# Kernel tuning notes

Hardware: AMD Instinct MI355X
Metric: run time of the kernel (lower is better)

The kernel has to match this reference:

```python
import jax, jax.numpy as jnp
import numpy as np

D_MODEL = 1024
NUM_HEADS = 16
D_K = D_MODEL // NUM_HEADS
THETA = 10000.0
B, T = 4, 2048


def apply_rope(x, positions):
    # x: [B, h, T, d_k], positions: [B, T] int
    half = D_K // 2
    inv_freq = 1.0 / (THETA ** (jnp.arange(half, dtype=jnp.float32) * 2.0 / D_K))  # [half]
    ang = positions.astype(jnp.float32)[:, None, :, None] * inv_freq  # [B,1,T,half]
    cos, sin = jnp.cos(ang), jnp.sin(ang)
    x1, x2 = x[..., 0::2], x[..., 1::2]  # even/odd interleaved pairs
    r1 = x1 * cos - x2 * sin
    r2 = x1 * sin + x2 * cos
    return jnp.stack([r1, r2], axis=-1).reshape(x.shape)


def setup_inputs() -> dict:
    key = jax.random.key(0)
    ks = jax.random.split(key, 5)
    scale = 1.0 / np.sqrt(D_MODEL)
    return {
        "in_features": jax.random.normal(ks[0], (B, T, D_MODEL), dtype=jnp.float32),
        "token_positions": jnp.broadcast_to(jnp.arange(T, dtype=jnp.int64), (B, T)),
        "Wq": jax.random.normal(ks[1], (D_MODEL, D_MODEL), dtype=jnp.float32) * scale,
        "Wk": jax.random.normal(ks[2], (D_MODEL, D_MODEL), dtype=jnp.float32) * scale,
        "Wv": jax.random.normal(ks[3], (D_MODEL, D_MODEL), dtype=jnp.float32) * scale,
        "Wo": jax.random.normal(ks[4], (D_MODEL, D_MODEL), dtype=jnp.float32) * scale,
    }


def reference(in_features, token_positions, Wq, Wk, Wv, Wo):
    x = in_features  # [B, T, d_model]
    # Linear stores weight [out, in]; y = x @ W.T (no bias)
    def proj(W):
        y = jnp.einsum('btd,ed->bte', x, W)
        return y.reshape(B, T, NUM_HEADS, D_K).transpose(0, 2, 1, 3)  # [B,h,T,d_k]
    Q, K, V = proj(Wq), proj(Wk), proj(Wv)
    Q = apply_rope(Q, token_positions)
    K = apply_rope(K, token_positions)
    scores = jnp.einsum('bhqd,bhkd->bhqk', Q, K) / jnp.sqrt(jnp.float32(D_K))
    causal = jnp.tril(jnp.ones((T, T), dtype=bool))  # True where allowed
    scores = jnp.where(causal, scores, jnp.float32(-1e30))
    attn = jax.nn.softmax(scores, axis=-1)
    heads = jnp.einsum('bhqk,bhkd->bhqd', attn, V)  # [B,h,T,d_k]
    out = heads.transpose(0, 2, 1, 3).reshape(B, T, D_MODEL)
    return jnp.einsum('btd,ed->bte', out, Wo)
```

## Files before the change

### kernel.cpp

```cpp
#include <hip/hip_runtime.h>
#include <cstdint>
#include <cstddef>

typedef unsigned short ushort_t;
typedef __attribute__((ext_vector_type(8))) short short8;
typedef __attribute__((ext_vector_type(4))) float f32x4;
typedef __attribute__((ext_vector_type(4))) _Float16 half4;
struct half4x2 { half4 lo, hi; };

__device__ __forceinline__ unsigned short f2bf(float f) {
    unsigned u = __float_as_uint(f);
    u += 0x7fffu + ((u >> 16) & 1u);
    return (unsigned short)(u >> 16);
}
__device__ __forceinline__ float bf2f(unsigned short h) {
    return __uint_as_float((unsigned)h << 16);
}
__device__ __forceinline__ ushort_t f2h(float f) {
    _Float16 h = (_Float16)f;
    return __builtin_bit_cast(unsigned short, h);
}
__device__ __forceinline__ f32x4 zero4() {
    f32x4 z; z[0]=0.f; z[1]=0.f; z[2]=0.f; z[3]=0.f; return z;
}
__device__ __forceinline__ void gld_lds16(const ushort_t* g, ushort_t* l) {
    __builtin_amdgcn_global_load_lds(
        (const __attribute__((address_space(1))) void*)g,
        (__attribute__((address_space(3))) void*)l, 16, 0, 0);
}

__global__ void cvt_all(const float* __restrict__ x,
                        const float* __restrict__ wq, const float* __restrict__ wk,
                        const float* __restrict__ wv, const float* __restrict__ wo,
                        ushort_t* __restrict__ xb,
                        ushort_t* __restrict__ wqb, ushort_t* __restrict__ wkb,
                        ushort_t* __restrict__ wvb, ushort_t* __restrict__ wob) {
    int idx = blockIdx.x * 256 + threadIdx.x;
    const float* src; ushort_t* dst; int off;
    if (idx < 2097152) { src = x; dst = xb; off = idx; }
    else {
        int r = idx - 2097152;
        int w = r >> 18;
        off = r & 262143;
        src = (w == 0) ? wq : (w == 1) ? wk : (w == 2) ? wv : wo;
        dst = (w == 0) ? wqb : (w == 1) ? wkb : (w == 2) ? wvb : wob;
    }
    float4 v = ((const float4*)src)[off];
    ushort_t o[4];
    o[0] = f2bf(v.x); o[1] = f2bf(v.y); o[2] = f2bf(v.z); o[3] = f2bf(v.w);
    *(ushort4*)(dst + 4*(size_t)off) = *(const ushort4*)o;
}

__device__ __forceinline__ void gemm_core(const ushort_t* __restrict__ A,
                                          const ushort_t* __restrict__ W,
                                          ushort_t* As, ushort_t* Bs,
                                          int m0, int n0, f32x4 (&acc)[4][4]) {
    const int tid  = threadIdx.x;
    const int wave = tid >> 6, lane = tid & 63;
    const int wm = (wave >> 1) * 64, wn = (wave & 1) * 64;
    const int lrow = lane >> 2, lcol = (lane & 3) * 8;
    const int q = lane >> 4, c = lane & 15;

    const ushort_t* ag0 = A + (size_t)(m0 + wave*16 + lrow) * 1024 + lcol;
    const ushort_t* ag1 = A + (size_t)(m0 + 64 + wave*16 + lrow) * 1024 + lcol;
    const ushort_t* bg0 = W + (size_t)(n0 + wave*16 + lrow) * 1024 + lcol;
    const ushort_t* bg1 = W + (size_t)(n0 + 64 + wave*16 + lrow) * 1024 + lcol;
    ushort_t* al0 = As + wave*512;
    ushort_t* al1 = As + 2048 + wave*512;
    ushort_t* bl0 = Bs + wave*512;
    ushort_t* bl1 = Bs + 2048 + wave*512;

    for (int k0 = 0; k0 < 1024; k0 += 32) {
        __syncthreads();
        gld_lds16(ag0 + k0, al0);
        gld_lds16(ag1 + k0, al1);
        gld_lds16(bg0 + k0, bl0);
        gld_lds16(bg1 + k0, bl1);
        asm volatile("s_waitcnt vmcnt(0)" ::: "memory");
        __syncthreads();

        short8 af[4], bf[4];
#pragma unroll
        for (int i = 0; i < 4; ++i)
            af[i] = *(const short8*)(As + (wm + i*16 + c)*32 + q*8);
#pragma unroll
        for (int j = 0; j < 4; ++j)
            bf[j] = *(const short8*)(Bs + (wn + j*16 + c)*32 + q*8);
#pragma unroll
        for (int i = 0; i < 4; ++i)
#pragma unroll
            for (int j = 0; j < 4; ++j)
                acc[i][j] = __builtin_amdgcn_mfma_f32_16x16x32_bf16(af[i], bf[j], acc[i][j], 0, 0, 0);
    }
}

__global__ __launch_bounds__(256) void gemm_qkv_kernel(
    const ushort_t* __restrict__ X, const ushort_t* __restrict__ Wq,
    const ushort_t* __restrict__ Wk, const ushort_t* __restrict__ Wv,
    ushort_t* __restrict__ Q, ushort_t* __restrict__ K, ushort_t* __restrict__ V) {
    __shared__ ushort_t As[128*32];
    __shared__ ushort_t Bs[128*32];
    const int which = blockIdx.z;
    const ushort_t* W = (which == 0) ? Wq : (which == 1) ? Wk : Wv;
    ushort_t* OUT    = (which == 0) ? Q  : (which == 1) ? K  : V;
    const int m0 = blockIdx.y * 128, n0 = blockIdx.x * 128;

    f32x4 acc[4][4];
#pragma unroll
    for (int i = 0; i < 4; ++i)
#pragma unroll
        for (int j = 0; j < 4; ++j) acc[i][j] = zero4();

    gemm_core(X, W, As, Bs, m0, n0, acc);

    const int lane = threadIdx.x & 63, wave = threadIdx.x >> 6;
    const int q = lane >> 4, c = lane & 15;
    const int wm = (wave >> 1) * 64, wn = (wave & 1) * 64;
#pragma unroll
    for (int i = 0; i < 4; ++i)
#pragma unroll
        for (int j = 0; j < 4; ++j)
#pragma unroll
            for (int r = 0; r < 4; ++r) {
                int mm = m0 + wm + i*16 + q*4 + r;
                int nn = n0 + wn + j*16 + c;
                int b = mm >> 11, t = mm & 2047;
                int h = nn >> 6,  d = nn & 63;
                OUT[((size_t)((b << 4) + h) * 2048 + t) * 64 + d] = f2bf(acc[i][j][r]);
            }
}

__global__ __launch_bounds__(256) void gemm_out_kernel(
    const ushort_t* __restrict__ A, const ushort_t* __restrict__ Wo,
    float* __restrict__ OUT) {
    __shared__ ushort_t As[128*32];
    __shared__ ushort_t Bs[128*32];
    const int m0 = blockIdx.y * 128, n0 = blockIdx.x * 128;

    f32x4 acc[4][4];
#pragma unroll
    for (int i = 0; i < 4; ++i)
#pragma unroll
        for (int j = 0; j < 4; ++j) acc[i][j] = zero4();

    gemm_core(A, Wo, As, Bs, m0, n0, acc);

    const int lane = threadIdx.x & 63, wave = threadIdx.x >> 6;
    const int q = lane >> 4, c = lane & 15;
    const int wm = (wave >> 1) * 64, wn = (wave & 1) * 64;
#pragma unroll
    for (int i = 0; i < 4; ++i)
#pragma unroll
        for (int j = 0; j < 4; ++j)
#pragma unroll
            for (int r = 0; r < 4; ++r) {
                int mm = m0 + wm + i*16 + q*4 + r;
                int nn = n0 + wn + j*16 + c;
                OUT[(size_t)mm * 1024 + nn] = acc[i][j][r];
            }
}

__global__ void rope_kernel(ushort_t* __restrict__ X, float scale) {
    int i = blockIdx.x * 256 + threadIdx.x;
    int p = i & 31;
    int t = (i >> 5) & 2047;
    float freq = __expf((float)p * -0.2878231366242557f);
    float sn, cs;
    sincosf((float)t * freq, &sn, &cs);
    ushort2 v = ((ushort2*)X)[i];
    float x1 = bf2f(v.x), x2 = bf2f(v.y);
    float r1 = (x1 * cs - x2 * sn) * scale;
    float r2 = (x1 * sn + x2 * cs) * scale;
    v.x = f2bf(r1); v.y = f2bf(r2);
    ((ushort2*)X)[i] = v;
}

__global__ void transpose_v(const ushort_t* __restrict__ V, ushort_t* __restrict__ Vt) {
    __shared__ ushort_t tile[64 * 65];
    const int bh = blockIdx.y;
    const int kb = blockIdx.x;
    const ushort_t* src = V + ((size_t)bh * 2048 + kb * 64) * 64;
    for (int f = threadIdx.x; f < 4096; f += 256) {
        tile[(f >> 6) * 65 + (f & 63)] = src[f];
    }
    __syncthreads();
    ushort_t* dst = Vt + ((size_t)bh * 32 + kb) * 4096;
    for (int f = threadIdx.x; f < 4096; f += 256) {
        int p = f >> 9, lane = (f >> 3) & 63, e = f & 7;
        int qq = lane >> 4, cc = lane & 15;
        int dj = p >> 1, jnp = p & 1;
        int jn = jnp * 2 + (e >> 2);
        int klocal = jn * 16 + qq * 4 + (e & 3);
        int d = dj * 16 + cc;
        dst[f] = f2h(bf2f(tile[klocal * 65 + d]));
    }
}

__global__ __launch_bounds__(256, 2) void flash_kernel(
    const ushort_t* __restrict__ Q, const ushort_t* __restrict__ K,
    const ushort_t* __restrict__ Vt, ushort_t* __restrict__ AO) {
    const int bh   = blockIdx.x;
    const int g    = blockIdx.y;
    const int wave = threadIdx.x >> 6, lane = threadIdx.x & 63;
    const int q = lane >> 4, c = lane & 15;
    const int i = g * 4 + wave;
    const int b = bh >> 4, h = bh & 15;

    const ushort_t* Qp = Q  + (size_t)bh * 131072;
    const ushort_t* Kp = K  + (size_t)bh * 131072;
    const ushort_t* Vp = Vt + (size_t)bh * 131072;

    const int chunks[2] = { i, 63 - i };

    auto loadK = [&](short8 (&kf)[4][2], int kb) {
#pragma unroll
        for (int jn = 0; jn < 4; ++jn) {
            const ushort_t* kp = Kp + (size_t)(kb * 64 + jn * 16 + c) * 64 + q * 8;
            kf[jn][0] = *(const short8*)kp;
            kf[jn][1] = *(const short8*)(kp + 32);
        }
    };
    auto loadV = [&](short8 (&va)[8], int kb) {
        const ushort_t* vp = Vp + (size_t)kb * 4096 + lane * 8;
#pragma unroll
        for (int p = 0; p < 8; ++p) va[p] = *(const short8*)(vp + p * 512);
    };

    for (int cc = 0; cc < 2; ++cc) {
        const int c0  = chunks[cc];
        const int qlo = c0 * 32;
        const int nt  = (c0 >> 1) + 1;

        short8 qf[2][2];
#pragma unroll
        for (int m = 0; m < 2; ++m)
#pragma unroll
            for (int ks = 0; ks < 2; ++ks)
                qf[m][ks] = *(const short8*)(Qp + (size_t)(qlo + m*16 + c) * 64 + ks * 32 + q * 8);

        f32x4 ot[2][4];
#pragma unroll
        for (int m = 0; m < 2; ++m)
#pragma unroll
            for (int dj = 0; dj < 4; ++dj) ot[m][dj] = zero4();
        float lpart[2] = {0.f, 0.f};

        auto compute = [&](short8 (&kf)[4][2], short8 (&va)[8], int kb) {
            f32x4 st[2][4];
#pragma unroll
            for (int m = 0; m < 2; ++m)
#pragma unroll
                for (int jn = 0; jn < 4; ++jn) {
                    f32x4 t0 = __builtin_amdgcn_mfma_f32_16x16x32_bf16(kf[jn][0], qf[m][0], zero4(), 0, 0, 0);
                    st[m][jn] = __builtin_amdgcn_mfma_f32_16x16x32_bf16(kf[jn][1], qf[m][1], t0, 0, 0, 0);
                }
            if (kb == nt - 1) {
#pragma unroll
                for (int m = 0; m < 2; ++m) {
                    int query = qlo + m * 16 + c;
#pragma unroll
                    for (int jn = 0; jn < 4; ++jn)
#pragma unroll
                        for (int r = 0; r < 4; ++r)
                            if (kb * 64 + jn * 16 + q * 4 + r > query) st[m][jn][r] = -1e30f;
                }
            }
            half4 pa[2][4];
#pragma unroll
            for (int m = 0; m < 2; ++m)
#pragma unroll
                for (int jn = 0; jn < 4; ++jn)
#pragma unroll
                    for (int r = 0; r < 4; ++r) {
                        float p = __expf(st[m][jn][r]);
                        lpart[m] += p;
                        pa[m][jn][r] = (_Float16)p;
                    }
#pragma unroll
            for (int jn = 0; jn < 4; ++jn)
#pragma unroll
                for (int dj = 0; dj < 4; ++dj) {
                    half4x2 vv = __builtin_bit_cast(half4x2, va[dj * 2 + (jn >> 1)]);
                    half4 vf = (jn & 1) ? vv.hi : vv.lo;
#pragma unroll
                    for (int m = 0; m < 2; ++m)
                        ot[m][dj] = __builtin_amdgcn_mfma_f32_16x16x16f16(vf, pa[m][jn], ot[m][dj], 0, 0, 0);
                }
        };

        short8 k0[4][2], k1[4][2], v0[8], v1[8];
        loadK(k0, 0); loadV(v0, 0);
        int kb = 0;
        while (true) {
            int nx = (kb + 1 < nt) ? kb + 1 : nt - 1;
            loadK(k1, nx); loadV(v1, nx);
            compute(k0, v0, kb);
            if (++kb >= nt) break;
            nx = (kb + 1 < nt) ? kb + 1 : nt - 1;
            loadK(k0, nx); loadV(v0, nx);
            compute(k1, v1, kb);
            if (++kb >= nt) break;
        }

#pragma unroll
        for (int m = 0; m < 2; ++m) {
            float l = lpart[m];
            l += __shfl_xor(l, 16);
            l += __shfl_xor(l, 32);
            float inv = 1.f / l;
            int t = qlo + m * 16 + c;
            ushort_t* base = AO + ((size_t)b * 2048 + t) * 1024 + h * 64;
#pragma unroll
            for (int dj = 0; dj < 4; ++dj) {
                ushort4 o;
                o.x = f2bf(ot[m][dj][0] * inv);
                o.y = f2bf(ot[m][dj][1] * inv);
                o.z = f2bf(ot[m][dj][2] * inv);
                o.w = f2bf(ot[m][dj][3] * inv);
                *(ushort4*)(base + dj * 16 + q * 4) = o;
            }
        }
    }
}

extern "C" void kernel_launch(void* const* d_in, const int* in_sizes, int n_in,
                              void* d_out, int out_size, void* d_ws, size_t ws_size,
                              hipStream_t stream) {
    const float* x  = (const float*)d_in[0];
    const float* Wq = (const float*)d_in[2];
    const float* Wk = (const float*)d_in[3];
    const float* Wv = (const float*)d_in[4];
    const float* Wo = (const float*)d_in[5];
    float* out = (float*)d_out;

    ushort_t* ws  = (ushort_t*)d_ws;
    ushort_t* Xb  = ws;
    ushort_t* Qb  = ws + 8388608;
    ushort_t* Kb  = ws + 16777216;
    ushort_t* Vb  = ws + 25165824;
    ushort_t* Vtb = ws + 33554432;
    ushort_t* Wqb = ws + 41943040;
    ushort_t* Wkb = Wqb + 1048576;
    ushort_t* Wvb = Wkb + 1048576;
    ushort_t* Wob = Wvb + 1048576;

    cvt_all<<<12288, 256, 0, stream>>>(x, Wq, Wk, Wv, Wo, Xb, Wqb, Wkb, Wvb, Wob);

    gemm_qkv_kernel<<<dim3(8, 64, 3), 256, 0, stream>>>(Xb, Wqb, Wkb, Wvb, Qb, Kb, Vb);

    rope_kernel<<<16384, 256, 0, stream>>>(Qb, 0.125f);
    rope_kernel<<<16384, 256, 0, stream>>>(Kb, 1.0f);

    transpose_v<<<dim3(32, 64), 256, 0, stream>>>(Vb, Vtb);

    flash_kernel<<<dim3(64, 8), 256, 0, stream>>>(Qb, Kb, Vtb, Xb);

    gemm_out_kernel<<<dim3(8, 64), 256, 0, stream>>>(Xb, Wob, out);
}
```

Measured before the change: 302.9 us.

## Fuse RoPE into QKV GEMM, widen GEMM K-tile with swizzle, split flash KV across waves

RoPE is now applied in the QKV GEMM epilogue. It uses a precomputed cos/sin table and a lane shuffle for the pair partner, which removes the two separate rope passes over Q and K. The GEMM core loads 64-wide K slices into XOR-swizzled LDS to halve barrier count and reduce bank conflicts. Flash attention is reorganised so each block handles one query chunk with two waves that split the KV tiles and combine their results through LDS. It also uses exp2 with a log2e-folded Q scale, packed fp16 conversion, and MFMA-based row sums. The table aliases the Vt buffer before transpose_v overwrites it, which is safe only because of launch ordering.

Result: slower. 520.1 us (+71.7%).

```diff
diff --git a/kernel.cpp b/kernel.cpp
--- a/kernel.cpp
+++ b/kernel.cpp
@@ -6,7 +6,10 @@
 typedef __attribute__((ext_vector_type(8))) short short8;
 typedef __attribute__((ext_vector_type(4))) float f32x4;
 typedef __attribute__((ext_vector_type(4))) _Float16 half4;
+typedef __attribute__((ext_vector_type(2))) _Float16 half2;
+typedef __attribute__((ext_vector_type(2))) __fp16 fp16v2;
 struct half4x2 { half4 lo, hi; };
+struct half2x2 { half2 lo, hi; };
 
 __device__ __forceinline__ unsigned short f2bf(float f) {
     unsigned u = __float_as_uint(f);
@@ -22,6 +25,12 @@
 }
 __device__ __forceinline__ f32x4 zero4() {
     f32x4 z; z[0]=0.f; z[1]=0.f; z[2]=0.f; z[3]=0.f; return z;
+}
+__device__ __forceinline__ half4 pk4(float a, float b, float cc, float d) {
+    half2x2 t;
+    t.lo = __builtin_bit_cast(half2, (fp16v2)__builtin_amdgcn_cvt_pkrtz(a, b));
+    t.hi = __builtin_bit_cast(half2, (fp16v2)__builtin_amdgcn_cvt_pkrtz(cc, d));
+    return __builtin_bit_cast(half4, t);
 }
 __device__ __forceinline__ void gld_lds16(const ushort_t* g, ushort_t* l) {
     __builtin_amdgcn_global_load_lds(
@@ -51,6 +60,15 @@
     *(ushort4*)(dst + 4*(size_t)off) = *(const ushort4*)o;
 }
 
+__global__ void rope_table(float2* __restrict__ tab) {
+    int i = blockIdx.x * 256 + threadIdx.x;
+    int t = i >> 5, p = i & 31;
+    float freq = __expf((float)p * -0.2878231366242557f);
+    float sn, cs;
+    sincosf((float)t * freq, &sn, &cs);
+    tab[i] = make_float2(cs, sn);
+}
+
 __device__ __forceinline__ void gemm_core(const ushort_t* __restrict__ A,
                                           const ushort_t* __restrict__ W,
                                           ushort_t* As, ushort_t* Bs,
@@ -58,48 +76,53 @@
     const int tid  = threadIdx.x;
     const int wave = tid >> 6, lane = tid & 63;
     const int wm = (wave >> 1) * 64, wn = (wave & 1) * 64;
-    const int lrow = lane >> 2, lcol = (lane & 3) * 8;
     const int q = lane >> 4, c = lane & 15;
-
-    const ushort_t* ag0 = A + (size_t)(m0 + wave*16 + lrow) * 1024 + lcol;
-    const ushort_t* ag1 = A + (size_t)(m0 + 64 + wave*16 + lrow) * 1024 + lcol;
-    const ushort_t* bg0 = W + (size_t)(n0 + wave*16 + lrow) * 1024 + lcol;
-    const ushort_t* bg1 = W + (size_t)(n0 + 64 + wave*16 + lrow) * 1024 + lcol;
-    ushort_t* al0 = As + wave*512;
-    ushort_t* al1 = As + 2048 + wave*512;
-    ushort_t* bl0 = Bs + wave*512;
-    ushort_t* bl1 = Bs + 2048 + wave*512;
-
-    for (int k0 = 0; k0 < 1024; k0 += 32) {
+    const int srow = lane >> 3;
+    const int gch  = (lane & 7) ^ srow;
+
+    const ushort_t* ag = A + (size_t)(m0 + wave*8 + srow) * 1024 + gch*8;
+    const ushort_t* bg = W + (size_t)(n0 + wave*8 + srow) * 1024 + gch*8;
+    ushort_t* al = As + wave*512;
+    ushort_t* bl = Bs + wave*512;
+
+    for (int k0 = 0; k0 < 1024; k0 += 64) {
         __syncthreads();
-        gld_lds16(ag0 + k0, al0);
-        gld_lds16(ag1 + k0, al1);
-        gld_lds16(bg0 + k0, bl0);
-        gld_lds16(bg1 + k0, bl1);
+#pragma unroll
+        for (int n = 0; n < 4; ++n) gld_lds16(ag + (size_t)n*32768 + k0, al + n*2048);
+#pragma unroll
+        for (int n = 0; n < 4; ++n) gld_lds16(bg + (size_t)n*32768 + k0, bl + n*2048);
         asm volatile("s_waitcnt vmcnt(0)" ::: "memory");
         __syncthreads();
 
-        short8 af[4], bf[4];
-#pragma unroll
-        for (int i = 0; i < 4; ++i)
-            af[i] = *(const short8*)(As + (wm + i*16 + c)*32 + q*8);
-#pragma unroll
-        for (int j = 0; j < 4; ++j)
-            bf[j] = *(const short8*)(Bs + (wn + j*16 + c)*32 + q*8);
-#pragma unroll
-        for (int i = 0; i < 4; ++i)
-#pragma unroll
-            for (int j = 0; j < 4; ++j)
-                acc[i][j] = __builtin_amdgcn_mfma_f32_16x16x32_bf16(af[i], bf[j], acc[i][j], 0, 0, 0);
+#pragma unroll
+        for (int sk = 0; sk < 2; ++sk) {
+            short8 af[4], bf[4];
+#pragma unroll
+            for (int i = 0; i < 4; ++i) {
+                int row = wm + i*16 + c;
+                af[i] = *(const short8*)(As + row*64 + (((sk*4 + q) ^ (row & 7)) * 8));
+            }
+#pragma unroll
+            for (int j = 0; j < 4; ++j) {
+                int row = wn + j*16 + c;
+                bf[j] = *(const short8*)(Bs + row*64 + (((sk*4 + q) ^ (row & 7)) * 8));
+            }
+#pragma unroll
+            for (int i = 0; i < 4; ++i)
+#pragma unroll
+                for (int j = 0; j < 4; ++j)
+                    acc[i][j] = __builtin_amdgcn_mfma_f32_16x16x32_bf16(af[i], bf[j], acc[i][j], 0, 0, 0);
+        }
     }
 }
 
 __global__ __launch_bounds__(256) void gemm_qkv_kernel(
     const ushort_t* __restrict__ X, const ushort_t* __restrict__ Wq,
     const ushort_t* __restrict__ Wk, const ushort_t* __restrict__ Wv,
+    const float2* __restrict__ tab,
     ushort_t* __restrict__ Q, ushort_t* __restrict__ K, ushort_t* __restrict__ V) {
-    __shared__ ushort_t As[128*32];
-    __shared__ ushort_t Bs[128*32];
+    __shared__ ushort_t As[128*64];
+    __shared__ ushort_t Bs[128*64];
     const int which = blockIdx.z;
     const ushort_t* W = (which == 0) ? Wq : (which == 1) ? Wk : Wv;
     ushort_t* OUT    = (which == 0) ? Q  : (which == 1) ? K  : V;
@@ -116,25 +139,37 @@
     const int lane = threadIdx.x & 63, wave = threadIdx.x >> 6;
     const int q = lane >> 4, c = lane & 15;
     const int wm = (wave >> 1) * 64, wn = (wave & 1) * 64;
+    const float scale = (which == 0) ? 0.18033688011112042f : 1.0f;
+    const bool dorope = (which < 2);
+
 #pragma unroll
     for (int i = 0; i < 4; ++i)
 #pragma unroll
-        for (int j = 0; j < 4; ++j)
+        for (int j = 0; j < 4; ++j) {
+            int nn = n0 + wn + j*16 + c;
+            int d = nn & 63, h = nn >> 6;
+            int pidx = d >> 1;
+            float sgn = (d & 1) ? 1.f : -1.f;
 #pragma unroll
             for (int r = 0; r < 4; ++r) {
                 int mm = m0 + wm + i*16 + q*4 + r;
-                int nn = n0 + wn + j*16 + c;
                 int b = mm >> 11, t = mm & 2047;
-                int h = nn >> 6,  d = nn & 63;
-                OUT[((size_t)((b << 4) + h) * 2048 + t) * 64 + d] = f2bf(acc[i][j][r]);
-            }
+                float val = acc[i][j][r];
+                if (dorope) {
+                    float partner = __shfl_xor(val, 1);
+                    float2 cs = tab[t * 32 + pidx];
+                    val = (val * cs.x + sgn * partner * cs.y) * scale;
+                }
+                OUT[((size_t)((b << 4) + h) * 2048 + t) * 64 + d] = f2bf(val);
+            }
+        }
 }
 
 __global__ __launch_bounds__(256) void gemm_out_kernel(
     const ushort_t* __restrict__ A, const ushort_t* __restrict__ Wo,
     float* __restrict__ OUT) {
-    __shared__ ushort_t As[128*32];
-    __shared__ ushort_t Bs[128*32];
+    __shared__ ushort_t As[128*64];
+    __shared__ ushort_t Bs[128*64];
     const int m0 = blockIdx.y * 128, n0 = blockIdx.x * 128;
 
     f32x4 acc[4][4];
@@ -158,21 +193,6 @@
                 int nn = n0 + wn + j*16 + c;
                 OUT[(size_t)mm * 1024 + nn] = acc[i][j][r];
             }
-}
-
-__global__ void rope_kernel(ushort_t* __restrict__ X, float scale) {
-    int i = blockIdx.x * 256 + threadIdx.x;
-    int p = i & 31;
-    int t = (i >> 5) & 2047;
-    float freq = __expf((float)p * -0.2878231366242557f);
-    float sn, cs;
-    sincosf((float)t * freq, &sn, &cs);
-    ushort2 v = ((ushort2*)X)[i];
-    float x1 = bf2f(v.x), x2 = bf2f(v.y);
-    float r1 = (x1 * cs - x2 * sn) * scale;
-    float r2 = (x1 * sn + x2 * cs) * scale;
-    v.x = f2bf(r1); v.y = f2bf(r2);
-    ((ushort2*)X)[i] = v;
 }
 
 __global__ void transpose_v(const ushort_t* __restrict__ V, ushort_t* __restrict__ Vt) {
@@ -196,21 +216,40 @@
     }
 }
 
-__global__ __launch_bounds__(256, 2) void flash_kernel(
+__global__ __launch_bounds__(128, 3) void flash_kernel(
     const ushort_t* __restrict__ Q, const ushort_t* __restrict__ K,
     const ushort_t* __restrict__ Vt, ushort_t* __restrict__ AO) {
-    const int bh   = blockIdx.x;
-    const int g    = blockIdx.y;
-    const int wave = threadIdx.x >> 6, lane = threadIdx.x & 63;
+    __shared__ float comb[64 * 34];
+    const int bh = blockIdx.x;
+    const int c0 = 63 - blockIdx.y;
+    const int h  = threadIdx.x >> 6, lane = threadIdx.x & 63;
     const int q = lane >> 4, c = lane & 15;
-    const int i = g * 4 + wave;
-    const int b = bh >> 4, h = bh & 15;
+    const int qlo = c0 * 32;
+    const int nt  = (c0 >> 1) + 1;
+    const int b = bh >> 4, hh = bh & 15;
 
     const ushort_t* Qp = Q  + (size_t)bh * 131072;
     const ushort_t* Kp = K  + (size_t)bh * 131072;
     const ushort_t* Vp = Vt + (size_t)bh * 131072;
 
-    const int chunks[2] = { i, 63 - i };
+    short8 qf[2][2];
+#pragma unroll
+    for (int m = 0; m < 2; ++m)
+#pragma unroll
+        for (int ks = 0; ks < 2; ++ks)
+            qf[m][ks] = *(const short8*)(Qp + (size_t)(qlo + m*16 + c) * 64 + ks * 32 + q * 8);
+
+    f32x4 ot[2][4];
+#pragma unroll
+    for (int m = 0; m < 2; ++m)
+#pragma unroll
+        for (int dj = 0; dj < 4; ++dj) ot[m][dj] = zero4();
+    f32x4 lacc[2];
+    lacc[0] = zero4(); lacc[1] = zero4();
+
+    half4 ones;
+#pragma unroll
+    for (int e = 0; e < 4; ++e) ones[e] = (_Float16)1.0f;
 
     auto loadK = [&](short8 (&kf)[4][2], int kb) {
 #pragma unroll
@@ -226,97 +265,93 @@
         for (int p = 0; p < 8; ++p) va[p] = *(const short8*)(vp + p * 512);
     };
 
-    for (int cc = 0; cc < 2; ++cc) {
-        const int c0  = chunks[cc];
-        const int qlo = c0 * 32;
-        const int nt  = (c0 >> 1) + 1;
-
-        short8 qf[2][2];
+    auto compute = [&](short8 (&kf)[4][2], short8 (&va)[8], int kb) {
+        f32x4 st[2][4];
 #pragma unroll
         for (int m = 0; m < 2; ++m)
 #pragma unroll
-            for (int ks = 0; ks < 2; ++ks)
-                qf[m][ks] = *(const short8*)(Qp + (size_t)(qlo + m*16 + c) * 64 + ks * 32 + q * 8);
-
-        f32x4 ot[2][4];
+            for (int jn = 0; jn < 4; ++jn) {
+                f32x4 t0 = __builtin_amdgcn_mfma_f32_16x16x32_bf16(kf[jn][0], qf[m][0], zero4(), 0, 0, 0);
+                st[m][jn] = __builtin_amdgcn_mfma_f32_16x16x32_bf16(kf[jn][1], qf[m][1], t0, 0, 0, 0);
+            }
+        if (kb == nt - 1) {
+#pragma unroll
+            for (int m = 0; m < 2; ++m) {
+                int query = qlo + m * 16 + c;
+#pragma unroll
+                for (int jn = 0; jn < 4; ++jn)
+#pragma unroll
+                    for (int r = 0; r < 4; ++r)
+                        if (kb * 64 + jn * 16 + q * 4 + r > query) st[m][jn][r] = -1e30f;
+            }
+        }
+        half4 pa[2][4];
 #pragma unroll
         for (int m = 0; m < 2; ++m)
 #pragma unroll
-            for (int dj = 0; dj < 4; ++dj) ot[m][dj] = zero4();
-        float lpart[2] = {0.f, 0.f};
-
-        auto compute = [&](short8 (&kf)[4][2], short8 (&va)[8], int kb) {
-            f32x4 st[2][4];
-#pragma unroll
-            for (int m = 0; m < 2; ++m)
-#pragma unroll
-                for (int jn = 0; jn < 4; ++jn) {
-                    f32x4 t0 = __builtin_amdgcn_mfma_f32_16x16x32_bf16(kf[jn][0], qf[m][0], zero4(), 0, 0, 0);
-                    st[m][jn] = __builtin_amdgcn_mfma_f32_16x16x32_bf16(kf[jn][1], qf[m][1], t0, 0, 0, 0);
-                }
-            if (kb == nt - 1) {
-#pragma unroll
-                for (int m = 0; m < 2; ++m) {
-                    int query = qlo + m * 16 + c;
-#pragma unroll
-                    for (int jn = 0; jn < 4; ++jn)
-#pragma unroll
-                        for (int r = 0; r < 4; ++r)
-                            if (kb * 64 + jn * 16 + q * 4 + r > query) st[m][jn][r] = -1e30f;
-                }
-            }
-            half4 pa[2][4];
-#pragma unroll
-            for (int m = 0; m < 2; ++m)
-#pragma unroll
-                for (int jn = 0; jn < 4; ++jn)
-#pragma unroll
-                    for (int r = 0; r < 4; ++r) {
-                        float p = __expf(st[m][jn][r]);
-                        lpart[m] += p;
-                        pa[m][jn][r] = (_Float16)p;
-                    }
-#pragma unroll
             for (int jn = 0; jn < 4; ++jn)
-#pragma unroll
-                for (int dj = 0; dj < 4; ++dj) {
-                    half4x2 vv = __builtin_bit_cast(half4x2, va[dj * 2 + (jn >> 1)]);
-                    half4 vf = (jn & 1) ? vv.hi : vv.lo;
-#pragma unroll
-                    for (int m = 0; m < 2; ++m)
-                        ot[m][dj] = __builtin_amdgcn_mfma_f32_16x16x16f16(vf, pa[m][jn], ot[m][dj], 0, 0, 0);
-                }
-        };
-
-        short8 k0[4][2], k1[4][2], v0[8], v1[8];
-        loadK(k0, 0); loadV(v0, 0);
-        int kb = 0;
-        while (true) {
-            int nx = (kb + 1 < nt) ? kb + 1 : nt - 1;
-            loadK(k1, nx); loadV(v1, nx);
-            compute(k0, v0, kb);
-            if (++kb >= nt) break;
-            nx = (kb + 1 < nt) ? kb + 1 : nt - 1;
-            loadK(k0, nx); loadV(v0, nx);
-            compute(k1, v1, kb);
-            if (++kb >= nt) break;
-        }
-
+                pa[m][jn] = pk4(exp2f(st[m][jn][0]), exp2f(st[m][jn][1]),
+                                exp2f(st[m][jn][2]), exp2f(st[m][jn][3]));
+#pragma unroll
+        for (int m = 0; m < 2; ++m)
+#pragma unroll
+            for (int jn = 0; jn < 4; ++jn)
+                lacc[m] = __builtin_amdgcn_mfma_f32_16x16x16f16(ones, pa[m][jn], lacc[m], 0, 0, 0);
+#pragma unroll
+        for (int jn = 0; jn < 4; ++jn)
+#pragma unroll
+            for (int dj = 0; dj < 4; ++dj) {
+                half4x2 vv = __builtin_bit_cast(half4x2, va[dj * 2 + (jn >> 1)]);
+                half4 vf = (jn & 1) ? vv.hi : vv.lo;
+#pragma unroll
+                for (int m = 0; m < 2; ++m)
+                    ot[m][dj] = __builtin_amdgcn_mfma_f32_16x16x16f16(vf, pa[m][jn], ot[m][dj], 0, 0, 0);
+            }
+    };
+
+    short8 k0[4][2], k1[4][2], v0[8], v1[8];
+    int kb = h;
+    if (kb < nt) { loadK(k0, kb); loadV(v0, kb); }
+    while (kb < nt) {
+        int nx = (kb + 2 < nt) ? kb + 2 : kb;
+        loadK(k1, nx); loadV(v1, nx);
+        compute(k0, v0, kb);
+        kb += 2;
+        if (kb >= nt) break;
+        nx = (kb + 2 < nt) ? kb + 2 : kb;
+        loadK(k0, nx); loadV(v0, nx);
+        compute(k1, v1, kb);
+        kb += 2;
+    }
+
+    if (h == 1) {
+        float* p = comb + lane * 34;
+#pragma unroll
+        for (int m = 0; m < 2; ++m)
+#pragma unroll
+            for (int dj = 0; dj < 4; ++dj)
+#pragma unroll
+                for (int r = 0; r < 4; ++r)
+                    p[m * 16 + dj * 4 + r] = ot[m][dj][r];
+        p[32] = lacc[0][0];
+        p[33] = lacc[1][0];
+    }
+    __syncthreads();
+    if (h == 0) {
+        const float* p = comb + lane * 34;
 #pragma unroll
         for (int m = 0; m < 2; ++m) {
-            float l = lpart[m];
-            l += __shfl_xor(l, 16);
-            l += __shfl_xor(l, 32);
+            float l = lacc[m][0] + p[32 + m];
             float inv = 1.f / l;
             int t = qlo + m * 16 + c;
-            ushort_t* base = AO + ((size_t)b * 2048 + t) * 1024 + h * 64;
+            ushort_t* base = AO + ((size_t)b * 2048 + t) * 1024 + hh * 64;
 #pragma unroll
             for (int dj = 0; dj < 4; ++dj) {
                 ushort4 o;
-                o.x = f2bf(ot[m][dj][0] * inv);
-                o.y = f2bf(ot[m][dj][1] * inv);
-                o.z = f2bf(ot[m][dj][2] * inv);
-                o.w = f2bf(ot[m][dj][3] * inv);
+                o.x = f2bf((ot[m][dj][0] + p[m*16 + dj*4 + 0]) * inv);
+                o.y = f2bf((ot[m][dj][1] + p[m*16 + dj*4 + 1]) * inv);
+                o.z = f2bf((ot[m][dj][2] + p[m*16 + dj*4 + 2]) * inv);
+                o.w = f2bf((ot[m][dj][3] + p[m*16 + dj*4 + 3]) * inv);
                 *(ushort4*)(base + dj * 16 + q * 4) = o;
             }
         }
@@ -343,17 +378,16 @@
     ushort_t* Wkb = Wqb + 1048576;
     ushort_t* Wvb = Wkb + 1048576;
     ushort_t* Wob = Wvb + 1048576;
+    float2* tab = (float2*)Vtb;
 
     cvt_all<<<12288, 256, 0, stream>>>(x, Wq, Wk, Wv, Wo, Xb, Wqb, Wkb, Wvb, Wob);
-
-    gemm_qkv_kernel<<<dim3(8, 64, 3), 256, 0, stream>>>(Xb, Wqb, Wkb, Wvb, Qb, Kb, Vb);
-
-    rope_kernel<<<16384, 256, 0, stream>>>(Qb, 0.125f);
-    rope_kernel<<<16384, 256, 0, stream>>>(Kb, 1.0f);
+    rope_table<<<256, 256, 0, stream>>>(tab);
+
+    gemm_qkv_kernel<<<dim3(8, 64, 3), 256, 0, stream>>>(Xb, Wqb, Wkb, Wvb, tab, Qb, Kb, Vb);
 
     transpose_v<<<dim3(32, 64), 256, 0, stream>>>(Vb, Vtb);
 
-    flash_kernel<<<dim3(64, 8), 256, 0, stream>>>(Qb, Kb, Vtb, Xb);
+    flash_kernel<<<dim3(64, 64), 128, 0, stream>>>(Qb, Kb, Vtb, Xb);
 
     gemm_out_kernel<<<dim3(8, 64), 256, 0, stream>>>(Xb, Wob, out);
 }
```
